# Kernel tuning notes

Hardware: AMD Instinct MI355X
Metric: run time of the kernel (lower is better)

The kernel has to match this reference:

```python
import jax, jax.numpy as jnp
import numpy as np

N_QUBITS = 8
N_Q_LAYERS = 4
TARGET = 0
B, N, H = 64, 512, 512


def _apply_1q(state, U, w):
    # apply 2x2 complex gate U on wire w of state with shape (2,)*n
    state = jnp.tensordot(U, state, axes=((1,), (w,)))
    return jnp.moveaxis(state, 0, w)


def _cnot(state, c, t):
    s0 = jnp.take(state, 0, axis=c)
    s1 = jnp.take(state, 1, axis=c)
    t_ = t - 1 if t > c else t
    s1 = jnp.flip(s1, axis=t_)  # X on target where control=1
    return jnp.stack([s0, s1], axis=c)


def _ry(theta):
    c, s = jnp.cos(theta / 2), jnp.sin(theta / 2)
    return jnp.stack([jnp.stack([c, -s]), jnp.stack([s, c])]).astype(jnp.complex64)


def _rx(theta):
    c, s = jnp.cos(theta / 2), jnp.sin(theta / 2)
    z = jnp.zeros_like(c)
    re = jnp.stack([jnp.stack([c, z]), jnp.stack([z, c])])
    im = jnp.stack([jnp.stack([z, s]), jnp.stack([s, z])])
    return (re.astype(jnp.complex64) - 1j * im.astype(jnp.complex64))


def _circuit(angles, weights):
    # AngleEmbedding(rotation='Y') + BasicEntanglerLayers(RX + CNOT ring) + <Z_i>
    n = N_QUBITS
    state = jnp.zeros((2,) * n, dtype=jnp.complex64).at[(0,) * n].set(1.0)
    for w in range(n):
        state = _apply_1q(state, _ry(angles[w]), w)
    for l in range(N_Q_LAYERS):
        for w in range(n):
            state = _apply_1q(state, _rx(weights[l, w]), w)
        for w in range(n):
            state = _cnot(state, w, (w + 1) % n)
    probs = state.real ** 2 + state.imag ** 2
    zs = []
    for i in range(n):
        p = probs.sum(axis=tuple(a for a in range(n) if a != i))  # [2]
        zs.append(p[0] - p[1])
    return jnp.stack(zs)  # [n_qubits]


def setup_inputs() -> dict:
    key = jax.random.key(0)
    ks = jax.random.split(key, 10)
    adj = jax.random.uniform(ks[1], (N, N), dtype=jnp.float32)
    norm_adj = adj / adj.sum(axis=1, keepdims=True)  # row-normalized adjacency
    sH = 1.0 / np.sqrt(H)
    return {
        "x": jax.random.normal(ks[0], (B, N, H), dtype=jnp.float32),
        "norm_adj": norm_adj,
        "W_gcn_w": jax.random.normal(ks[2], (H, H), dtype=jnp.float32) * sH,
        "W_gcn_b": jax.random.normal(ks[3], (H,), dtype=jnp.float32) * sH,
        "pre_w": jax.random.normal(ks[4], (N_QUBITS, H), dtype=jnp.float32) * sH,
        "pre_b": jax.random.normal(ks[5], (N_QUBITS,), dtype=jnp.float32) * sH,
        "post_w": jax.random.normal(ks[6], (H, N_QUBITS), dtype=jnp.float32) * (1.0 / np.sqrt(N_QUBITS)),
        "post_b": jax.random.normal(ks[7], (H,), dtype=jnp.float32) * (1.0 / np.sqrt(N_QUBITS)),
        "q_weights": jax.random.uniform(ks[8], (N_Q_LAYERS, N_QUBITS), dtype=jnp.float32) * 2.0 * jnp.pi,
    }


def reference(x, norm_adj, W_gcn_w, W_gcn_b, pre_w, pre_b, post_w, post_b, q_weights):
    # classical GCN aggregation over all N nodes
    x_agg = jnp.einsum('ij,bjh->bih', norm_adj, x)  # [B,N,H]
    x_agg = jax.nn.gelu(x_agg @ W_gcn_w.T + W_gcn_b, approximate=False)
    # dropout is identity in eval mode
    tgt = x_agg[:, TARGET, :]  # [B,H]
    x_qin = jnp.tanh(tgt @ pre_w.T + pre_b) * jnp.pi  # [B,n_qubits]
    q_out = jax.vmap(lambda a: _circuit(a, q_weights))(x_qin)  # [B,n_qubits]
    q_out = q_out @ post_w.T + post_b  # [B,H]
    out = x_agg.at[:, TARGET, :].set(q_out)
    return out
```

## Files before the change

kernel.cpp:

```cpp
#include <hip/hip_runtime.h>
#include <hip/hip_bf16.h>
#include <math.h>

#define B_  64
#define D_  512
#define NQ  8
#define NL  4

typedef __bf16 bf16;
typedef float  f32x4  __attribute__((ext_vector_type(4)));
typedef bf16   bf16x8 __attribute__((ext_vector_type(8)));

__device__ __forceinline__ void async_load16(const bf16* g, bf16* l) {
    __builtin_amdgcn_global_load_lds(
        (const __attribute__((address_space(1))) void*)g,
        (__attribute__((address_space(3))) void*)l, 16, 0, 0);
}

__global__ __launch_bounds__(256) void convert_kernel(const float* __restrict__ src,
                                                      bf16* __restrict__ dst, int n8) {
    int i = blockIdx.x * 256 + threadIdx.x;
    if (i < n8) {
        const float4 v0 = *(const float4*)(src + (size_t)i * 8);
        const float4 v1 = *(const float4*)(src + (size_t)i * 8 + 4);
        bf16x8 p;
        p[0] = (bf16)v0.x; p[1] = (bf16)v0.y; p[2] = (bf16)v0.z; p[3] = (bf16)v0.w;
        p[4] = (bf16)v1.x; p[5] = (bf16)v1.y; p[6] = (bf16)v1.z; p[7] = (bf16)v1.w;
        *(bf16x8*)(dst + (size_t)i * 8) = p;
    }
}

template <int GELU>
__global__ __launch_bounds__(256) void gemm_nt_dma(const bf16* __restrict__ A,
                                                   const bf16* __restrict__ Bv,
                                                   const float* __restrict__ bias,
                                                   void* __restrict__ Cout) {
    __shared__ bf16 As[128 * 64];
    __shared__ bf16 Bs[128 * 64];
    const int b    = blockIdx.y;
    const int tile = blockIdx.x;
    const int m0   = (tile >> 2) * 128;
    const int n0   = (tile & 3) * 128;
    const int t    = threadIdx.x;
    const int lane = t & 63;
    const int w    = t >> 6;
    const int wr   = (w >> 1) * 64;
    const int wc   = (w & 1) * 64;
    const int l15  = lane & 15;
    const int quad = lane >> 4;

    f32x4 acc[4][4];
    for (int i = 0; i < 4; i++)
        for (int j = 0; j < 4; j++) acc[i][j] = (f32x4)(0.0f);

    const bf16* Bb = Bv + (size_t)b * D_ * D_;

    const int rl = lane >> 3;
    const int ck = (lane & 7) ^ rl;

    for (int k0 = 0; k0 < D_; k0 += 64) {
        #pragma unroll
        for (int j = 0; j < 4; j++) {
            int rbase = w * 32 + j * 8;
            async_load16(A  + (size_t)(m0 + rbase + rl) * D_ + k0 + ck * 8, &As[rbase * 64]);
            async_load16(Bb + (size_t)(n0 + rbase + rl) * D_ + k0 + ck * 8, &Bs[rbase * 64]);
        }
        __syncthreads();
        #pragma unroll
        for (int kk = 0; kk < 2; kk++) {
            bf16x8 af[4], bfr[4];
            #pragma unroll
            for (int mt = 0; mt < 4; mt++) {
                int row = wr + mt * 16 + l15;
                int s   = (kk * 4 + quad) ^ (l15 & 7);
                af[mt] = *(const bf16x8*)&As[row * 64 + s * 8];
            }
            #pragma unroll
            for (int nt = 0; nt < 4; nt++) {
                int row = wc + nt * 16 + l15;
                int s   = (kk * 4 + quad) ^ (l15 & 7);
                bfr[nt] = *(const bf16x8*)&Bs[row * 64 + s * 8];
            }
            #pragma unroll
            for (int mt = 0; mt < 4; mt++)
                #pragma unroll
                for (int nt = 0; nt < 4; nt++)
                    acc[mt][nt] = __builtin_amdgcn_mfma_f32_16x16x32_bf16(af[mt], bfr[nt], acc[mt][nt], 0, 0, 0);
        }
        __syncthreads();
    }

    if (GELU == 0) {
        bf16* Cb = (bf16*)Cout + (size_t)b * D_ * D_;
        for (int mt = 0; mt < 4; mt++) {
            int row = m0 + wr + mt * 16 + quad * 4;
            for (int nt = 0; nt < 4; nt++) {
                int col = n0 + wc + nt * 16 + l15;
                for (int r = 0; r < 4; r++)
                    Cb[(size_t)(row + r) * D_ + col] = (bf16)acc[mt][nt][r];
            }
        }
    } else {
        float* Cb = (float*)Cout + (size_t)b * D_ * D_;
        for (int mt = 0; mt < 4; mt++) {
            int row = m0 + wr + mt * 16 + quad * 4;
            for (int nt = 0; nt < 4; nt++) {
                int col = n0 + wc + nt * 16 + l15;
                float bv = bias[col];
                for (int r = 0; r < 4; r++) {
                    float v = acc[mt][nt][r] + bv;
                    Cb[(size_t)(row + r) * D_ + col] = 0.5f * v * (1.0f + erff(v * 0.70710678118654752f));
                }
            }
        }
    }
}

#define PITCH 40
template <int GELU>
__global__ __launch_bounds__(256) void gemm_nt_legacy(const float* __restrict__ A,
                                                      const bf16* __restrict__ Bv,
                                                      const float* __restrict__ bias,
                                                      void* __restrict__ Cout) {
    __shared__ bf16 As[128 * PITCH];
    __shared__ bf16 Bs[128 * 32];
    const int b    = blockIdx.y;
    const int tile = blockIdx.x;
    const int m0   = (tile >> 2) * 128;
    const int n0   = (tile & 3) * 128;
    const int t    = threadIdx.x;
    const int lane = t & 63;
    const int w    = t >> 6;
    const int wr   = (w >> 1) * 64;
    const int wc   = (w & 1) * 64;
    const int l15  = lane & 15;
    const int quad = lane >> 4;

    f32x4 acc[4][4];
    for (int i = 0; i < 4; i++)
        for (int j = 0; j < 4; j++) acc[i][j] = (f32x4)(0.0f);

    const bf16* Bb = Bv + (size_t)b * D_ * D_;

    for (int k0 = 0; k0 < D_; k0 += 32) {
        for (int c = t; c < 512; c += 256) {
            int row = c >> 2, ch = c & 3;
            const float* s = A + (size_t)(m0 + row) * D_ + k0 + ch * 8;
            const float4 v0 = *(const float4*)s;
            const float4 v1 = *(const float4*)(s + 4);
            bf16x8 p;
            p[0] = (bf16)v0.x; p[1] = (bf16)v0.y; p[2] = (bf16)v0.z; p[3] = (bf16)v0.w;
            p[4] = (bf16)v1.x; p[5] = (bf16)v1.y; p[6] = (bf16)v1.z; p[7] = (bf16)v1.w;
            *(bf16x8*)&As[row * PITCH + ch * 8] = p;
        }
        {
            int rl = lane >> 2;
            int kchunk = (lane & 3) ^ ((lane >> 3) & 3);
            #pragma unroll
            for (int j = 0; j < 2; j++) {
                int rbase = w * 32 + j * 16;
                async_load16(Bb + (size_t)(n0 + rbase + rl) * D_ + k0 + kchunk * 8, &Bs[rbase * 32]);
            }
        }
        __syncthreads();
        bf16x8 af[4], bfr[4];
        #pragma unroll
        for (int mt = 0; mt < 4; mt++)
            af[mt] = *(const bf16x8*)&As[(wr + mt * 16 + l15) * PITCH + quad * 8];
        #pragma unroll
        for (int nt = 0; nt < 4; nt++) {
            int row = wc + nt * 16 + l15;
            int kx  = quad ^ ((l15 >> 1) & 3);
            bfr[nt] = *(const bf16x8*)&Bs[row * 32 + kx * 8];
        }
        #pragma unroll
        for (int mt = 0; mt < 4; mt++)
            #pragma unroll
            for (int nt = 0; nt < 4; nt++)
                acc[mt][nt] = __builtin_amdgcn_mfma_f32_16x16x32_bf16(af[mt], bfr[nt], acc[mt][nt], 0, 0, 0);
        __syncthreads();
    }

    if (GELU == 0) {
        bf16* Cb = (bf16*)Cout + (size_t)b * D_ * D_;
        for (int mt = 0; mt < 4; mt++) {
            int row = m0 + wr + mt * 16 + quad * 4;
            for (int nt = 0; nt < 4; nt++) {
                int col = n0 + wc + nt * 16 + l15;
                for (int r = 0; r < 4; r++)
                    Cb[(size_t)(row + r) * D_ + col] = (bf16)acc[mt][nt][r];
            }
        }
    } else {
        float* Cb = (float*)Cout + (size_t)b * D_ * D_;
        for (int mt = 0; mt < 4; mt++) {
            int row = m0 + wr + mt * 16 + quad * 4;
            for (int nt = 0; nt < 4; nt++) {
                int col = n0 + wc + nt * 16 + l15;
                float bv = bias[col];
                for (int r = 0; r < 4; r++) {
                    float v = acc[mt][nt][r] + bv;
                    Cb[(size_t)(row + r) * D_ + col] = 0.5f * v * (1.0f + erff(v * 0.70710678118654752f));
                }
            }
        }
    }
}

__global__ __launch_bounds__(64) void quantum_kernel(float* __restrict__ out,
                                                     const float* __restrict__ pre_w,
                                                     const float* __restrict__ pre_b,
                                                     const float* __restrict__ post_w,
                                                     const float* __restrict__ post_b,
                                                     const float* __restrict__ qw) {
    const int b = blockIdx.x;
    const int l = threadIdx.x;
    float* row0 = out + (size_t)b * D_ * D_;

    float tg[8];
    #pragma unroll
    for (int j = 0; j < 8; j++) tg[j] = row0[l + 64 * j];

    float ang[NQ];
    #pragma unroll
    for (int q = 0; q < NQ; q++) {
        float s = 0.f;
        #pragma unroll
        for (int j = 0; j < 8; j++) s += tg[j] * pre_w[q * D_ + l + 64 * j];
        #pragma unroll
        for (int m = 32; m >= 1; m >>= 1) s += __shfl_xor(s, m, 64);
        ang[q] = tanhf(s + pre_b[q]) * 3.14159265358979323846f;
    }

    float cw[NQ], sw[NQ];
    #pragma unroll
    for (int w = 0; w < NQ; w++) { cw[w] = cosf(0.5f * ang[w]); sw[w] = sinf(0.5f * ang[w]); }
    float re[4], im[4];
    #pragma unroll
    for (int r = 0; r < 4; r++) {
        int idx = l * 4 + r;
        float a = 1.f;
        #pragma unroll
        for (int w = 0; w < NQ; w++) a *= ((idx >> (7 - w)) & 1) ? sw[w] : cw[w];
        re[r] = a; im[r] = 0.f;
    }

    for (int lay = 0; lay < NL; lay++) {
        #pragma unroll
        for (int w = 0; w < 6; w++) {
            float th = 0.5f * qw[lay * NQ + w];
            float c = cosf(th), s = sinf(th);
            int m = 1 << (5 - w);
            #pragma unroll
            for (int r = 0; r < 4; r++) {
                float pre_ = __shfl_xor(re[r], m, 64);
                float pim_ = __shfl_xor(im[r], m, 64);
                re[r] = c * re[r] + s * pim_;
                im[r] = c * im[r] - s * pre_;
            }
        }
        {
            float th = 0.5f * qw[lay * NQ + 6];
            float c = cosf(th), s = sinf(th);
            float or0 = re[0], or1 = re[1], or2 = re[2], or3 = re[3];
            float oi0 = im[0], oi1 = im[1], oi2 = im[2], oi3 = im[3];
            re[0] = c * or0 + s * oi2;  im[0] = c * oi0 - s * or2;
            re[1] = c * or1 + s * oi3;  im[1] = c * oi1 - s * or3;
            re[2] = c * or2 + s * oi0;  im[2] = c * oi2 - s * or0;
            re[3] = c * or3 + s * oi1;  im[3] = c * oi3 - s * or1;
        }
        {
            float th = 0.5f * qw[lay * NQ + 7];
            float c = cosf(th), s = sinf(th);
            float or0 = re[0], or1 = re[1], or2 = re[2], or3 = re[3];
            float oi0 = im[0], oi1 = im[1], oi2 = im[2], oi3 = im[3];
            re[0] = c * or0 + s * oi1;  im[0] = c * oi0 - s * or1;
            re[1] = c * or1 + s * oi0;  im[1] = c * oi1 - s * or0;
            re[2] = c * or2 + s * oi3;  im[2] = c * oi2 - s * or3;
            re[3] = c * or3 + s * oi2;  im[3] = c * oi3 - s * or2;
        }
        #pragma unroll
        for (int w = 0; w < 5; w++) {
            int cb = 7 - w, tb = 6 - w;
            int tm = 1 << (tb - 2);
            bool ctl = (l >> (cb - 2)) & 1;
            #pragma unroll
            for (int r = 0; r < 4; r++) {
                float pre_ = __shfl_xor(re[r], tm, 64);
                float pim_ = __shfl_xor(im[r], tm, 64);
                re[r] = ctl ? pre_ : re[r];
                im[r] = ctl ? pim_ : im[r];
            }
        }
        {
            bool ctl = l & 1;
            float t0 = re[0], t1 = re[1], t2 = re[2], t3 = re[3];
            float u0 = im[0], u1 = im[1], u2 = im[2], u3 = im[3];
            re[0] = ctl ? t2 : t0;  re[1] = ctl ? t3 : t1;
            re[2] = ctl ? t0 : t2;  re[3] = ctl ? t1 : t3;
            im[0] = ctl ? u2 : u0;  im[1] = ctl ? u3 : u1;
            im[2] = ctl ? u0 : u2;  im[3] = ctl ? u1 : u3;
        }
        {
            float t2 = re[2], t3 = re[3], u2 = im[2], u3 = im[3];
            re[2] = t3; re[3] = t2; im[2] = u3; im[3] = u2;
        }
        {
            #pragma unroll
            for (int r = 0; r < 4; r++) {
                float pre_ = __shfl_xor(re[r], 32, 64);
                float pim_ = __shfl_xor(im[r], 32, 64);
                if (r & 1) { re[r] = pre_; im[r] = pim_; }
            }
        }
    }

    float pr[4];
    #pragma unroll
    for (int r = 0; r < 4; r++) pr[r] = re[r] * re[r] + im[r] * im[r];
    float z[NQ];
    #pragma unroll
    for (int q = 0; q < NQ; q++) {
        int bit = 7 - q;
        float s = 0.f;
        #pragma unroll
        for (int r = 0; r < 4; r++) {
            int idx = l * 4 + r;
            s += ((idx >> bit) & 1) ? -pr[r] : pr[r];
        }
        #pragma unroll
        for (int m = 32; m >= 1; m >>= 1) s += __shfl_xor(s, m, 64);
        z[q] = s;
    }

    #pragma unroll
    for (int j = 0; j < 8; j++) {
        int h = l + 64 * j;
        float v = post_b[h];
        #pragma unroll
        for (int q = 0; q < NQ; q++) v += z[q] * post_w[h * NQ + q];
        row0[h] = v;
    }
}

extern "C" void kernel_launch(void* const* d_in, const int* in_sizes, int n_in,
                              void* d_out, int out_size, void* d_ws, size_t ws_size,
                              hipStream_t stream) {
    const float* x        = (const float*)d_in[0];
    const float* norm_adj = (const float*)d_in[1];
    const float* W_gcn_w  = (const float*)d_in[2];
    const float* W_gcn_b  = (const float*)d_in[3];
    const float* pre_w    = (const float*)d_in[4];
    const float* pre_b    = (const float*)d_in[5];
    const float* post_w   = (const float*)d_in[6];
    const float* post_b   = (const float*)d_in[7];
    const float* q_w      = (const float*)d_in[8];
    float* out = (float*)d_out;

    bf16* xbf = (bf16*)d_out;
    bf16* Yt  = (bf16*)d_ws;

    const int n8_x = B_ * D_ * D_ / 8;
    const int n8_m = D_ * D_ / 8;
    convert_kernel<<<(n8_x + 255) / 256, 256, 0, stream>>>(x, xbf, n8_x);

    dim3 grid(16, B_);
    const size_t MB32 = (size_t)32 * 1024 * 1024;
    if (ws_size >= MB32 + 2 * 1024 * 1024) {
        bf16* Wbf   = (bf16*)((char*)d_ws + MB32);
        bf16* adjbf = Wbf + D_ * D_;
        convert_kernel<<<(n8_m + 255) / 256, 256, 0, stream>>>(W_gcn_w, Wbf, n8_m);
        convert_kernel<<<(n8_m + 255) / 256, 256, 0, stream>>>(norm_adj, adjbf, n8_m);
        gemm_nt_dma<0><<<grid, 256, 0, stream>>>(Wbf, xbf, nullptr, (void*)Yt);
        gemm_nt_dma<1><<<grid, 256, 0, stream>>>(adjbf, Yt, W_gcn_b, (void*)out);
    } else {
        gemm_nt_legacy<0><<<grid, 256, 0, stream>>>(W_gcn_w, xbf, nullptr, (void*)Yt);
        gemm_nt_legacy<1><<<grid, 256, 0, stream>>>(norm_adj, Yt, W_gcn_b, (void*)out);
    }

    quantum_kernel<<<B_, 64, 0, stream>>>(out, pre_w, pre_b, post_w, post_b, q_w);
}
```

Before: 207.6 us.

## Double-buffer GEMM K-loop, remap blocks per XCD, fuse weight conversions

After: 215.8 us. 1.04x slower.

```diff
diff --git a/kernel.cpp b/kernel.cpp
--- a/kernel.cpp
+++ b/kernel.cpp
@@ -30,17 +30,38 @@
     }
 }
 
+__global__ __launch_bounds__(256) void convert2_kernel(const float* __restrict__ s0,
+                                                       const float* __restrict__ s1,
+                                                       bf16* __restrict__ dst, int n8each) {
+    int i = blockIdx.x * 256 + threadIdx.x;
+    if (i < 2 * n8each) {
+        const float* s = (i < n8each) ? (s0 + (size_t)i * 8)
+                                      : (s1 + (size_t)(i - n8each) * 8);
+        const float4 v0 = *(const float4*)s;
+        const float4 v1 = *(const float4*)(s + 4);
+        bf16x8 p;
+        p[0] = (bf16)v0.x; p[1] = (bf16)v0.y; p[2] = (bf16)v0.z; p[3] = (bf16)v0.w;
+        p[4] = (bf16)v1.x; p[5] = (bf16)v1.y; p[6] = (bf16)v1.z; p[7] = (bf16)v1.w;
+        *(bf16x8*)(dst + (size_t)i * 8) = p;
+    }
+}
+
 template <int GELU>
 __global__ __launch_bounds__(256) void gemm_nt_dma(const bf16* __restrict__ A,
                                                    const bf16* __restrict__ Bv,
                                                    const float* __restrict__ bias,
                                                    void* __restrict__ Cout) {
-    __shared__ bf16 As[128 * 64];
-    __shared__ bf16 Bs[128 * 64];
-    const int b    = blockIdx.y;
-    const int tile = blockIdx.x;
+    __shared__ bf16 As[2][128 * 32];
+    __shared__ bf16 Bs[2][128 * 32];
+
+    const int flat = blockIdx.y * 16 + blockIdx.x;
+    const int xcd  = flat & 7;
+    const int idx  = flat >> 3;
+    const int b    = (xcd << 3) | (idx >> 4);
+    const int tile = idx & 15;
     const int m0   = (tile >> 2) * 128;
     const int n0   = (tile & 3) * 128;
+
     const int t    = threadIdx.x;
     const int lane = t & 63;
     const int w    = t >> 6;
@@ -55,38 +76,49 @@
 
     const bf16* Bb = Bv + (size_t)b * D_ * D_;
 
-    const int rl = lane >> 3;
-    const int ck = (lane & 7) ^ rl;
-
-    for (int k0 = 0; k0 < D_; k0 += 64) {
-        #pragma unroll
-        for (int j = 0; j < 4; j++) {
-            int rbase = w * 32 + j * 8;
-            async_load16(A  + (size_t)(m0 + rbase + rl) * D_ + k0 + ck * 8, &As[rbase * 64]);
-            async_load16(Bb + (size_t)(n0 + rbase + rl) * D_ + k0 + ck * 8, &Bs[rbase * 64]);
-        }
-        __syncthreads();
-        #pragma unroll
-        for (int kk = 0; kk < 2; kk++) {
-            bf16x8 af[4], bfr[4];
-            #pragma unroll
-            for (int mt = 0; mt < 4; mt++) {
-                int row = wr + mt * 16 + l15;
-                int s   = (kk * 4 + quad) ^ (l15 & 7);
-                af[mt] = *(const bf16x8*)&As[row * 64 + s * 8];
-            }
-            #pragma unroll
-            for (int nt = 0; nt < 4; nt++) {
-                int row = wc + nt * 16 + l15;
-                int s   = (kk * 4 + quad) ^ (l15 & 7);
-                bfr[nt] = *(const bf16x8*)&Bs[row * 64 + s * 8];
-            }
-            #pragma unroll
-            for (int mt = 0; mt < 4; mt++)
-                #pragma unroll
-                for (int nt = 0; nt < 4; nt++)
-                    acc[mt][nt] = __builtin_amdgcn_mfma_f32_16x16x32_bf16(af[mt], bfr[nt], acc[mt][nt], 0, 0, 0);
-        }
+    const int rl = lane >> 2;
+    const int ck = (lane & 3) ^ ((lane >> 3) & 3);
+
+    #pragma unroll
+    for (int j = 0; j < 2; j++) {
+        const int rbase = w * 32 + j * 16;
+        async_load16(A  + (size_t)(m0 + rbase + rl) * D_ + ck * 8, &As[0][rbase * 32]);
+        async_load16(Bb + (size_t)(n0 + rbase + rl) * D_ + ck * 8, &Bs[0][rbase * 32]);
+    }
+    __syncthreads();
+
+    #pragma unroll
+    for (int s = 0; s < 16; s++) {
+        const int p = s & 1;
+        if (s < 15) {
+            const int k0 = (s + 1) * 32;
+            #pragma unroll
+            for (int j = 0; j < 2; j++) {
+                const int rbase = w * 32 + j * 16;
+                async_load16(A  + (size_t)(m0 + rbase + rl) * D_ + k0 + ck * 8,
+                             &As[p ^ 1][rbase * 32]);
+                async_load16(Bb + (size_t)(n0 + rbase + rl) * D_ + k0 + ck * 8,
+                             &Bs[p ^ 1][rbase * 32]);
+            }
+        }
+        bf16x8 af[4], bfr[4];
+        #pragma unroll
+        for (int mt = 0; mt < 4; mt++) {
+            const int row = wr + mt * 16 + l15;
+            const int sl  = quad ^ ((l15 >> 1) & 3);
+            af[mt] = *(const bf16x8*)&As[p][row * 32 + sl * 8];
+        }
+        #pragma unroll
+        for (int nt = 0; nt < 4; nt++) {
+            const int row = wc + nt * 16 + l15;
+            const int sl  = quad ^ ((l15 >> 1) & 3);
+            bfr[nt] = *(const bf16x8*)&Bs[p][row * 32 + sl * 8];
+        }
+        #pragma unroll
+        for (int mt = 0; mt < 4; mt++)
+            #pragma unroll
+            for (int nt = 0; nt < 4; nt++)
+                acc[mt][nt] = __builtin_amdgcn_mfma_f32_16x16x32_bf16(af[mt], bfr[nt], acc[mt][nt], 0, 0, 0);
         __syncthreads();
     }
 
@@ -369,8 +401,7 @@
     if (ws_size >= MB32 + 2 * 1024 * 1024) {
         bf16* Wbf   = (bf16*)((char*)d_ws + MB32);
         bf16* adjbf = Wbf + D_ * D_;
-        convert_kernel<<<(n8_m + 255) / 256, 256, 0, stream>>>(W_gcn_w, Wbf, n8_m);
-        convert_kernel<<<(n8_m + 255) / 256, 256, 0, stream>>>(norm_adj, adjbf, n8_m);
+        convert2_kernel<<<(2 * n8_m + 255) / 256, 256, 0, stream>>>(W_gcn_w, norm_adj, Wbf, n8_m);
         gemm_nt_dma<0><<<grid, 256, 0, stream>>>(Wbf, xbf, nullptr, (void*)Yt);
         gemm_nt_dma<1><<<grid, 256, 0, stream>>>(adjbf, Yt, W_gcn_b, (void*)out);
     } else {
```
